# Kernel tuning notes

Measured on AMD Instinct MI355X. Metric: run time of the kernel, lower is better.

## Reference

```python
import jax, jax.numpy as jnp
import numpy as np

DEFAULT_MASK_VALUE = -0.7 * float(jnp.finfo(jnp.dtype('float32')).max)

B, T, NQ, NKV, D = 2, 1024, 32, 8, 128


def setup_inputs() -> dict:
    key = jax.random.key(0)
    k1, k2, k3, k4 = jax.random.split(key, 4)
    query = jax.random.normal(k1, (B, T, NQ, D), dtype=jnp.float32)
    kk = jax.random.normal(k2, (B, T, NKV, D), dtype=jnp.float32)
    vv = jax.random.normal(k3, (B, T, NKV, D), dtype=jnp.float32)
    # packed-sequence segment ids, sorted so each segment is contiguous (values 1..3, >0 = active)
    decoder_segment_ids = jnp.sort(jax.random.randint(k4, (B, T), 1, 4), axis=-1).astype(jnp.int32)
    return {"query": query, "key": kk, "value": vv,
            "decoder_segment_ids": decoder_segment_ids}


def _attention(query, key, value, decoder_segment_ids):
    # MaxText AttentionOp.apply_attention_dot (prefill / train mode), GQA layout.
    b, t, n, d = query.shape
    n_kv = key.shape[2]
    g = n // n_kv
    q = query.reshape(b, t, n_kv, g, d)
    # qk product: [b, n_kv, g, t, s]
    logits = jnp.einsum('btkgd,bskd->bkgts', q, key)
    # generate_attention_mask: segment mask AND causal mask
    seg_mask = decoder_segment_ids[:, :, None] == decoder_segment_ids[:, None, :]  # [b,t,s]
    row_ids = jax.lax.broadcasted_iota(jnp.int32, (t, t), 0)
    col_ids = jax.lax.broadcasted_iota(jnp.int32, (t, t), 1)
    causal = col_ids <= row_ids  # [t,s]
    mask = jnp.logical_and(seg_mask, causal[None])  # [b,t,s]
    # apply_mask_to_logits: replace masked entries with DEFAULT_MASK_VALUE (avoids add fusion)
    masked = jnp.where(mask[:, None, None, :, :], logits, DEFAULT_MASK_VALUE)
    probs = jax.nn.softmax(masked, axis=-1)
    out = jnp.einsum('bkgts,bskd->btkgd', probs, value)
    return out.reshape(b, t, n, d)


def reference(query, key, value, decoder_segment_ids):
    return _attention(query, key, value, decoder_segment_ids)
```

## Files before the change

kernel.cpp:

```cpp
#include <hip/hip_runtime.h>

constexpr int B_  = 2;
constexpr int T_  = 1024;
constexpr int NQ  = 32;
constexpr int NKV = 8;
constexpr int D_  = 128;

constexpr int BM = 64;
constexpr int BN = 64;
constexpr int NTILE = T_ / BM;
constexpr float MASK_NEG = -3.0e38f;

typedef _Float16 f16;
typedef f16 f16x2 __attribute__((ext_vector_type(2)));
typedef f16 f16x4 __attribute__((ext_vector_type(4)));
typedef f16 f16x8 __attribute__((ext_vector_type(8)));
typedef float floatx4 __attribute__((ext_vector_type(4)));

__global__ __launch_bounds__(256)
void fa_kernel(const float* __restrict__ Qg, const float* __restrict__ Kg,
               const float* __restrict__ Vg, const int* __restrict__ seg,
               float* __restrict__ Og) {
    __shared__ f16 lds_k[BN][136];
    __shared__ f16 lds_vt[D_][72];
    __shared__ f16 lds_p[4][16][72];
    __shared__ int lds_seg[T_];

    const int pair = blockIdx.x;
    const int h    = blockIdx.y;
    const int b    = blockIdx.z;
    const int kv   = h >> 2;

    const int tid  = threadIdx.x;
    const int wave = tid >> 6;
    const int lane = tid & 63;
    const int quad = lane >> 4;
    const int ln   = lane & 15;

    const int kd4 = tid & 31, kr8 = tid >> 5;
    const int vd  = tid & 127, vhalf = tid >> 7;

    const int* segb = seg + b * T_;
    *(int4*)&lds_seg[tid * 4] = *(const int4*)(segb + tid * 4);
    __syncthreads();

    for (int sub = 0; sub < 2; ++sub) {
        const int tile = sub ? pair : (NTILE - 1 - pair);
        const int t0 = tile * BM;

        const int qrow = t0 + wave * 16 + ln;
        const float* qptr = Qg + (((size_t)b * T_ + qrow) * NQ + h) * D_;
        f16x8 qfrag[4];
#pragma unroll
        for (int c = 0; c < 4; ++c) {
            const float* p = qptr + c * 32 + quad * 8;
            float4 f0 = *(const float4*)(p);
            float4 f1 = *(const float4*)(p + 4);
            f16x8 v;
            v[0] = (f16)f0.x; v[1] = (f16)f0.y; v[2] = (f16)f0.z; v[3] = (f16)f0.w;
            v[4] = (f16)f1.x; v[5] = (f16)f1.y; v[6] = (f16)f1.z; v[7] = (f16)f1.w;
            qfrag[c] = v;
        }

        int trow[4], segq[4];
#pragma unroll
        for (int r = 0; r < 4; ++r) {
            trow[r] = t0 + wave * 16 + quad * 4 + r;
            segq[r] = lds_seg[trow[r]];
        }
        const int seg_lo = lds_seg[t0];

        unsigned long long bal = __ballot(lds_seg[lane * 16 + 15] < seg_lo);
        const int blk_start = __popcll(bal) >> 2;
        const int nblk = tile + 1;

        float  m_i[4], l_i[4];
        floatx4 o_acc[8];
#pragma unroll
        for (int r = 0; r < 4; ++r) { m_i[r] = -1.0e30f; l_i[r] = 0.0f; }
#pragma unroll
        for (int dt = 0; dt < 8; ++dt) o_acc[dt] = floatx4{0.f, 0.f, 0.f, 0.f};

        float4 kreg[8];
        float  vreg[32];
        {
            const int s0 = blk_start * BN;
            const float* kb = Kg + (((size_t)b * T_ + s0 + kr8) * NKV + kv) * D_ + kd4 * 4;
#pragma unroll
            for (int i = 0; i < 8; ++i)
                kreg[i] = *(const float4*)(kb + (size_t)(8 * i) * NKV * D_);
            const float* vb = Vg + (((size_t)b * T_ + s0 + vhalf * 32) * NKV + kv) * D_ + vd;
#pragma unroll
            for (int i = 0; i < 32; ++i)
                vreg[i] = vb[(size_t)i * NKV * D_];
        }

        for (int blk = blk_start; blk < nblk; ++blk) {
            const int s0 = blk * BN;
            __syncthreads();

#pragma unroll
            for (int i = 0; i < 8; ++i) {
                f16x4 w;
                w[0] = (f16)kreg[i].x; w[1] = (f16)kreg[i].y;
                w[2] = (f16)kreg[i].z; w[3] = (f16)kreg[i].w;
                *(f16x4*)&lds_k[kr8 + 8 * i][kd4 * 4] = w;
            }
#pragma unroll
            for (int i = 0; i < 16; ++i) {
                f16x2 w; w[0] = (f16)vreg[2 * i]; w[1] = (f16)vreg[2 * i + 1];
                *(f16x2*)&lds_vt[vd][vhalf * 32 + 2 * i] = w;
            }
            __syncthreads();

            if (blk + 1 < nblk) {
                const int s0n = s0 + BN;
                const float* kb = Kg + (((size_t)b * T_ + s0n + kr8) * NKV + kv) * D_ + kd4 * 4;
#pragma unroll
                for (int i = 0; i < 8; ++i)
                    kreg[i] = *(const float4*)(kb + (size_t)(8 * i) * NKV * D_);
                const float* vb = Vg + (((size_t)b * T_ + s0n + vhalf * 32) * NKV + kv) * D_ + vd;
#pragma unroll
                for (int i = 0; i < 32; ++i)
                    vreg[i] = vb[(size_t)i * NKV * D_];
            }

            floatx4 sc[4];
#pragma unroll
            for (int nt = 0; nt < 4; ++nt) {
                floatx4 acc = floatx4{0.f, 0.f, 0.f, 0.f};
#pragma unroll
                for (int c = 0; c < 4; ++c) {
                    f16x8 kf = *(const f16x8*)&lds_k[nt * 16 + ln][c * 32 + quad * 8];
                    acc = __builtin_amdgcn_mfma_f32_16x16x32_f16(qfrag[c], kf, acc, 0, 0, 0);
                }
                sc[nt] = acc;
            }

#pragma unroll
            for (int nt = 0; nt < 4; ++nt) {
                const int s = s0 + nt * 16 + ln;
                const int sgs = lds_seg[s];
#pragma unroll
                for (int r = 0; r < 4; ++r) {
                    const bool ok = (s <= trow[r]) && (sgs == segq[r]);
                    sc[nt][r] = ok ? sc[nt][r] : MASK_NEG;
                }
            }

#pragma unroll
            for (int r = 0; r < 4; ++r) {
                float mx = fmaxf(fmaxf(sc[0][r], sc[1][r]), fmaxf(sc[2][r], sc[3][r]));
                mx = fmaxf(mx, __shfl_xor(mx, 1));
                mx = fmaxf(mx, __shfl_xor(mx, 2));
                mx = fmaxf(mx, __shfl_xor(mx, 4));
                mx = fmaxf(mx, __shfl_xor(mx, 8));
                const float mnew  = fmaxf(m_i[r], mx);
                const float alpha = __expf(m_i[r] - mnew);
                m_i[r] = mnew;
                float p0 = __expf(sc[0][r] - mnew);
                float p1 = __expf(sc[1][r] - mnew);
                float p2 = __expf(sc[2][r] - mnew);
                float p3 = __expf(sc[3][r] - mnew);
                sc[0][r] = p0; sc[1][r] = p1; sc[2][r] = p2; sc[3][r] = p3;
                float sm = (p0 + p1) + (p2 + p3);
                sm += __shfl_xor(sm, 1);
                sm += __shfl_xor(sm, 2);
                sm += __shfl_xor(sm, 4);
                sm += __shfl_xor(sm, 8);
                l_i[r] = l_i[r] * alpha + sm;
#pragma unroll
                for (int dt = 0; dt < 8; ++dt) o_acc[dt][r] *= alpha;
            }

#pragma unroll
            for (int nt = 0; nt < 4; ++nt)
#pragma unroll
                for (int r = 0; r < 4; ++r)
                    lds_p[wave][quad * 4 + r][nt * 16 + ln] = (f16)sc[nt][r];

            __builtin_amdgcn_s_waitcnt(0xc07f);

            f16x8 af0 = *(const f16x8*)&lds_p[wave][ln][quad * 8];
            f16x8 af1 = *(const f16x8*)&lds_p[wave][ln][32 + quad * 8];

#pragma unroll
            for (int dt = 0; dt < 8; ++dt) {
                f16x8 b0 = *(const f16x8*)&lds_vt[dt * 16 + ln][quad * 8];
                f16x8 b1 = *(const f16x8*)&lds_vt[dt * 16 + ln][32 + quad * 8];
                o_acc[dt] = __builtin_amdgcn_mfma_f32_16x16x32_f16(af0, b0, o_acc[dt], 0, 0, 0);
                o_acc[dt] = __builtin_amdgcn_mfma_f32_16x16x32_f16(af1, b1, o_acc[dt], 0, 0, 0);
            }
        }

#pragma unroll
        for (int r = 0; r < 4; ++r) {
            const float inv = 1.0f / l_i[r];
            float* optr = Og + (((size_t)b * T_ + trow[r]) * NQ + h) * D_ + ln;
#pragma unroll
            for (int dt = 0; dt < 8; ++dt)
                optr[dt * 16] = o_acc[dt][r] * inv;
        }
    }
}

extern "C" void kernel_launch(void* const* d_in, const int* in_sizes, int n_in,
                              void* d_out, int out_size, void* d_ws, size_t ws_size,
                              hipStream_t stream) {
    const float* Q   = (const float*)d_in[0];
    const float* K   = (const float*)d_in[1];
    const float* V   = (const float*)d_in[2];
    const int*   seg = (const int*)d_in[3];
    float* out = (float*)d_out;
    dim3 grid(NTILE / 2, NQ, B_);
    fa_kernel<<<grid, 256, 0, stream>>>(Q, K, V, seg, out);
}
```

Measured before the change: 131.0 us.

## Pre-convert K/V to fp16 with transposed V and double-buffer LDS tiles

Adds a prep kernel that converts K to fp16 and V to a transposed fp16 layout in global scratch. The attention kernel then loads these compactly into double-buffered LDS, which halves global traffic and removes per-block conversion and per-block syncs. The row-sum is computed by an extra MFMA against a ones vector instead of shuffle reductions. Segment ids are now read from global memory instead of LDS. The cost is a second kernel launch and extra scratch traffic, plus more LDS use.

Result: slower. 168.8 us (+28.9%).

```diff
diff --git a/kernel.cpp b/kernel.cpp
--- a/kernel.cpp
+++ b/kernel.cpp
@@ -12,19 +12,59 @@
 constexpr float MASK_NEG = -3.0e38f;
 
 typedef _Float16 f16;
-typedef f16 f16x2 __attribute__((ext_vector_type(2)));
 typedef f16 f16x4 __attribute__((ext_vector_type(4)));
 typedef f16 f16x8 __attribute__((ext_vector_type(8)));
 typedef float floatx4 __attribute__((ext_vector_type(4)));
 
+__device__ __align__(16) f16 g_K16 [(size_t)B_ * NKV * T_ * D_];
+__device__ __align__(16) f16 g_Vt16[(size_t)B_ * NKV * T_ * D_];
+
 __global__ __launch_bounds__(256)
-void fa_kernel(const float* __restrict__ Qg, const float* __restrict__ Kg,
-               const float* __restrict__ Vg, const int* __restrict__ seg,
+void prep_kernel(const float* __restrict__ K, const float* __restrict__ V) {
+    __shared__ f16 lv[64][136];
+    const int sblk = blockIdx.x;
+    const int kv   = blockIdx.y;
+    const int b    = blockIdx.z;
+    const int tid  = threadIdx.x;
+    const int s0   = sblk * 64;
+    const size_t inbase = ((size_t)b * T_) * NKV * D_ + (size_t)kv * D_;
+
+    f16* kout = g_K16 + ((size_t)(b * NKV + kv) * T_ + s0) * D_;
+#pragma unroll
+    for (int p = 0; p < 8; ++p) {
+        const int u = tid + 256 * p;
+        const int s = u >> 5, d4 = u & 31;
+        float4 f = *(const float4*)(K + inbase + (size_t)(s0 + s) * NKV * D_ + d4 * 4);
+        f16x4 hh; hh[0] = (f16)f.x; hh[1] = (f16)f.y; hh[2] = (f16)f.z; hh[3] = (f16)f.w;
+        *(f16x4*)(kout + s * D_ + d4 * 4) = hh;
+    }
+#pragma unroll
+    for (int p = 0; p < 8; ++p) {
+        const int u = tid + 256 * p;
+        const int s = u >> 5, d4 = u & 31;
+        float4 f = *(const float4*)(V + inbase + (size_t)(s0 + s) * NKV * D_ + d4 * 4);
+        f16x4 hh; hh[0] = (f16)f.x; hh[1] = (f16)f.y; hh[2] = (f16)f.z; hh[3] = (f16)f.w;
+        *(f16x4*)&lv[s][d4 * 4] = hh;
+    }
+    __syncthreads();
+    f16* vout = g_Vt16 + (size_t)((b * NKV + kv) * 16 + sblk) * 128 * 64;
+#pragma unroll
+    for (int p = 0; p < 4; ++p) {
+        const int u = tid + 256 * p;
+        const int d = u >> 3, cu = u & 7;
+        f16x8 hh;
+#pragma unroll
+        for (int j = 0; j < 8; ++j) hh[j] = lv[cu * 8 + j][d];
+        *(f16x8*)(vout + d * 64 + cu * 8) = hh;
+    }
+}
+
+__global__ __launch_bounds__(256, 2)
+void fa_kernel(const float* __restrict__ Qg, const int* __restrict__ seg,
                float* __restrict__ Og) {
-    __shared__ f16 lds_k[BN][136];
-    __shared__ f16 lds_vt[D_][72];
+    __shared__ f16 lds_k[2][BN][136];
+    __shared__ f16 lds_vt[2][D_][72];
     __shared__ f16 lds_p[4][16][72];
-    __shared__ int lds_seg[T_];
 
     const int pair = blockIdx.x;
     const int h    = blockIdx.y;
@@ -37,12 +77,13 @@
     const int quad = lane >> 4;
     const int ln   = lane & 15;
 
-    const int kd4 = tid & 31, kr8 = tid >> 5;
-    const int vd  = tid & 127, vhalf = tid >> 7;
-
     const int* segb = seg + b * T_;
-    *(int4*)&lds_seg[tid * 4] = *(const int4*)(segb + tid * 4);
-    __syncthreads();
+    const f16* kbase = g_K16 + (size_t)(b * NKV + kv) * T_ * D_;
+    const f16* vbase = g_Vt16 + (size_t)(b * NKV + kv) * 16 * 128 * 64;
+
+    f16x8 vones;
+#pragma unroll
+    for (int j = 0; j < 8; ++j) vones[j] = (f16)1.0f;
 
     for (int sub = 0; sub < 2; ++sub) {
         const int tile = sub ? pair : (NTILE - 1 - pair);
@@ -66,64 +107,59 @@
 #pragma unroll
         for (int r = 0; r < 4; ++r) {
             trow[r] = t0 + wave * 16 + quad * 4 + r;
-            segq[r] = lds_seg[trow[r]];
-        }
-        const int seg_lo = lds_seg[t0];
-
-        unsigned long long bal = __ballot(lds_seg[lane * 16 + 15] < seg_lo);
+            segq[r] = segb[trow[r]];
+        }
+        const int seg_lo = segb[t0];
+
+        unsigned long long bal = __ballot(segb[lane * 16 + 15] < seg_lo);
         const int blk_start = __popcll(bal) >> 2;
         const int nblk = tile + 1;
 
-        float  m_i[4], l_i[4];
-        floatx4 o_acc[8];
-#pragma unroll
-        for (int r = 0; r < 4; ++r) { m_i[r] = -1.0e30f; l_i[r] = 0.0f; }
-#pragma unroll
-        for (int dt = 0; dt < 8; ++dt) o_acc[dt] = floatx4{0.f, 0.f, 0.f, 0.f};
-
-        float4 kreg[8];
-        float  vreg[32];
+        float  m_i[4];
+        floatx4 o_acc[9];
+#pragma unroll
+        for (int r = 0; r < 4; ++r) m_i[r] = -1.0e30f;
+#pragma unroll
+        for (int dt = 0; dt < 9; ++dt) o_acc[dt] = floatx4{0.f, 0.f, 0.f, 0.f};
+
+        uint4 kst[4], vst[4];
         {
-            const int s0 = blk_start * BN;
-            const float* kb = Kg + (((size_t)b * T_ + s0 + kr8) * NKV + kv) * D_ + kd4 * 4;
-#pragma unroll
-            for (int i = 0; i < 8; ++i)
-                kreg[i] = *(const float4*)(kb + (size_t)(8 * i) * NKV * D_);
-            const float* vb = Vg + (((size_t)b * T_ + s0 + vhalf * 32) * NKV + kv) * D_ + vd;
-#pragma unroll
-            for (int i = 0; i < 32; ++i)
-                vreg[i] = vb[(size_t)i * NKV * D_];
-        }
-
+            const f16* kp = kbase + (size_t)blk_start * BN * D_;
+            const f16* vp = vbase + (size_t)blk_start * 128 * 64;
+#pragma unroll
+            for (int p = 0; p < 4; ++p) kst[p] = *(const uint4*)(kp + (tid + 256 * p) * 8);
+#pragma unroll
+            for (int p = 0; p < 4; ++p) vst[p] = *(const uint4*)(vp + (tid + 256 * p) * 8);
+        }
+        __syncthreads();
+#pragma unroll
+        for (int p = 0; p < 4; ++p) {
+            const int u = tid + 256 * p;
+            *(uint4*)&lds_k[0][u >> 4][(u & 15) * 8] = kst[p];
+        }
+#pragma unroll
+        for (int p = 0; p < 4; ++p) {
+            const int u = tid + 256 * p;
+            *(uint4*)&lds_vt[0][u >> 3][(u & 7) * 8] = vst[p];
+        }
+
+        int buf = 0;
         for (int blk = blk_start; blk < nblk; ++blk) {
             const int s0 = blk * BN;
             __syncthreads();
 
-#pragma unroll
-            for (int i = 0; i < 8; ++i) {
-                f16x4 w;
-                w[0] = (f16)kreg[i].x; w[1] = (f16)kreg[i].y;
-                w[2] = (f16)kreg[i].z; w[3] = (f16)kreg[i].w;
-                *(f16x4*)&lds_k[kr8 + 8 * i][kd4 * 4] = w;
-            }
-#pragma unroll
-            for (int i = 0; i < 16; ++i) {
-                f16x2 w; w[0] = (f16)vreg[2 * i]; w[1] = (f16)vreg[2 * i + 1];
-                *(f16x2*)&lds_vt[vd][vhalf * 32 + 2 * i] = w;
-            }
-            __syncthreads();
-
-            if (blk + 1 < nblk) {
-                const int s0n = s0 + BN;
-                const float* kb = Kg + (((size_t)b * T_ + s0n + kr8) * NKV + kv) * D_ + kd4 * 4;
-#pragma unroll
-                for (int i = 0; i < 8; ++i)
-                    kreg[i] = *(const float4*)(kb + (size_t)(8 * i) * NKV * D_);
-                const float* vb = Vg + (((size_t)b * T_ + s0n + vhalf * 32) * NKV + kv) * D_ + vd;
-#pragma unroll
-                for (int i = 0; i < 32; ++i)
-                    vreg[i] = vb[(size_t)i * NKV * D_];
-            }
+            const bool more = (blk + 1 < nblk);
+            if (more) {
+                const f16* kp = kbase + (size_t)(blk + 1) * BN * D_;
+                const f16* vp = vbase + (size_t)(blk + 1) * 128 * 64;
+#pragma unroll
+                for (int p = 0; p < 4; ++p) kst[p] = *(const uint4*)(kp + (tid + 256 * p) * 8);
+#pragma unroll
+                for (int p = 0; p < 4; ++p) vst[p] = *(const uint4*)(vp + (tid + 256 * p) * 8);
+            }
+            int segs[4];
+#pragma unroll
+            for (int nt = 0; nt < 4; ++nt) segs[nt] = segb[s0 + nt * 16 + ln];
 
             floatx4 sc[4];
 #pragma unroll
@@ -131,7 +167,7 @@
                 floatx4 acc = floatx4{0.f, 0.f, 0.f, 0.f};
 #pragma unroll
                 for (int c = 0; c < 4; ++c) {
-                    f16x8 kf = *(const f16x8*)&lds_k[nt * 16 + ln][c * 32 + quad * 8];
+                    f16x8 kf = *(const f16x8*)&lds_k[buf][nt * 16 + ln][c * 32 + quad * 8];
                     acc = __builtin_amdgcn_mfma_f32_16x16x32_f16(qfrag[c], kf, acc, 0, 0, 0);
                 }
                 sc[nt] = acc;
@@ -140,14 +176,14 @@
 #pragma unroll
             for (int nt = 0; nt < 4; ++nt) {
                 const int s = s0 + nt * 16 + ln;
-                const int sgs = lds_seg[s];
 #pragma unroll
                 for (int r = 0; r < 4; ++r) {
-                    const bool ok = (s <= trow[r]) && (sgs == segq[r]);
+                    const bool ok = (s <= trow[r]) && (segs[nt] == segq[r]);
                     sc[nt][r] = ok ? sc[nt][r] : MASK_NEG;
                 }
             }
 
+            floatx4 av;
 #pragma unroll
             for (int r = 0; r < 4; ++r) {
                 float mx = fmaxf(fmaxf(sc[0][r], sc[1][r]), fmaxf(sc[2][r], sc[3][r]));
@@ -155,23 +191,16 @@
                 mx = fmaxf(mx, __shfl_xor(mx, 2));
                 mx = fmaxf(mx, __shfl_xor(mx, 4));
                 mx = fmaxf(mx, __shfl_xor(mx, 8));
-                const float mnew  = fmaxf(m_i[r], mx);
-                const float alpha = __expf(m_i[r] - mnew);
+                const float mnew = fmaxf(m_i[r], mx);
+                av[r] = __expf(m_i[r] - mnew);
                 m_i[r] = mnew;
-                float p0 = __expf(sc[0][r] - mnew);
-                float p1 = __expf(sc[1][r] - mnew);
-                float p2 = __expf(sc[2][r] - mnew);
-                float p3 = __expf(sc[3][r] - mnew);
-                sc[0][r] = p0; sc[1][r] = p1; sc[2][r] = p2; sc[3][r] = p3;
-                float sm = (p0 + p1) + (p2 + p3);
-                sm += __shfl_xor(sm, 1);
-                sm += __shfl_xor(sm, 2);
-                sm += __shfl_xor(sm, 4);
-                sm += __shfl_xor(sm, 8);
-                l_i[r] = l_i[r] * alpha + sm;
-#pragma unroll
-                for (int dt = 0; dt < 8; ++dt) o_acc[dt][r] *= alpha;
-            }
+                sc[0][r] = __expf(sc[0][r] - mnew);
+                sc[1][r] = __expf(sc[1][r] - mnew);
+                sc[2][r] = __expf(sc[2][r] - mnew);
+                sc[3][r] = __expf(sc[3][r] - mnew);
+            }
+#pragma unroll
+            for (int dt = 0; dt < 9; ++dt) o_acc[dt] *= av;
 
 #pragma unroll
             for (int nt = 0; nt < 4; ++nt)
@@ -184,18 +213,36 @@
             f16x8 af0 = *(const f16x8*)&lds_p[wave][ln][quad * 8];
             f16x8 af1 = *(const f16x8*)&lds_p[wave][ln][32 + quad * 8];
 
+            if (more) {
+                const int ob = buf ^ 1;
+#pragma unroll
+                for (int p = 0; p < 4; ++p) {
+                    const int u = tid + 256 * p;
+                    *(uint4*)&lds_k[ob][u >> 4][(u & 15) * 8] = kst[p];
+                }
+#pragma unroll
+                for (int p = 0; p < 4; ++p) {
+                    const int u = tid + 256 * p;
+                    *(uint4*)&lds_vt[ob][u >> 3][(u & 7) * 8] = vst[p];
+                }
+            }
+
 #pragma unroll
             for (int dt = 0; dt < 8; ++dt) {
-                f16x8 b0 = *(const f16x8*)&lds_vt[dt * 16 + ln][quad * 8];
-                f16x8 b1 = *(const f16x8*)&lds_vt[dt * 16 + ln][32 + quad * 8];
+                f16x8 b0 = *(const f16x8*)&lds_vt[buf][dt * 16 + ln][quad * 8];
+                f16x8 b1 = *(const f16x8*)&lds_vt[buf][dt * 16 + ln][32 + quad * 8];
                 o_acc[dt] = __builtin_amdgcn_mfma_f32_16x16x32_f16(af0, b0, o_acc[dt], 0, 0, 0);
                 o_acc[dt] = __builtin_amdgcn_mfma_f32_16x16x32_f16(af1, b1, o_acc[dt], 0, 0, 0);
             }
+            o_acc[8] = __builtin_amdgcn_mfma_f32_16x16x32_f16(af0, vones, o_acc[8], 0, 0, 0);
+            o_acc[8] = __builtin_amdgcn_mfma_f32_16x16x32_f16(af1, vones, o_acc[8], 0, 0, 0);
+
+            buf ^= 1;
         }
 
 #pragma unroll
         for (int r = 0; r < 4; ++r) {
-            const float inv = 1.0f / l_i[r];
+            const float inv = 1.0f / o_acc[8][r];
             float* optr = Og + (((size_t)b * T_ + trow[r]) * NQ + h) * D_ + ln;
 #pragma unroll
             for (int dt = 0; dt < 8; ++dt)
@@ -212,6 +259,10 @@
     const float* V   = (const float*)d_in[2];
     const int*   seg = (const int*)d_in[3];
     float* out = (float*)d_out;
+
+    dim3 pgrid(NTILE, NKV, B_);
+    prep_kernel<<<pgrid, 256, 0, stream>>>(K, V);
+
     dim3 grid(NTILE / 2, NQ, B_);
-    fa_kernel<<<grid, 256, 0, stream>>>(Q, K, V, seg, out);
+    fa_kernel<<<grid, 256, 0, stream>>>(Q, seg, out);
 }
```
